# Optimization experiments

Measured on AMD Instinct MI355X. Metric: run time of the kernel, lower is better.

## Reference

```python
import jax, jax.numpy as jnp
import numpy as np

HIDDEN = 1024
HEADS = 16
HEAD_DIM = HIDDEN // HEADS
SCALE = HEAD_DIM ** (-0.5)


def setup_inputs() -> dict:
    key = jax.random.key(0)
    ks = jax.random.split(key, 5)
    B, N, C = 8, 1024, HIDDEN
    x = jax.random.normal(ks[0], (B, N, C), dtype=jnp.float32)
    # torch nn.Linear params: weight [out, in], bias [out]
    w_in = jax.random.normal(ks[1], (3 * C, C), dtype=jnp.float32) * (C ** -0.5)
    b_in = jax.random.normal(ks[2], (3 * C,), dtype=jnp.float32) * 0.02
    w_out = jax.random.normal(ks[3], (C, C), dtype=jnp.float32) * (C ** -0.5)
    b_out = jax.random.normal(ks[4], (C,), dtype=jnp.float32) * 0.02
    return {"x": x, "w_in": w_in, "b_in": b_in, "w_out": w_out, "b_out": b_out}


def reference(x, w_in, b_in, w_out, b_out):
    B, N, C = x.shape
    H, D = HEADS, HEAD_DIM
    # in_proj: [B,N,3C] -> (3,B,H,N,D)
    qkv = x @ w_in.T + b_in
    qkv = qkv.reshape(B, N, 3, H, D).transpose(2, 0, 3, 1, 4)
    q, k, v = qkv[0], qkv[1], qkv[2]
    # attention scores scaled after QK^T (same math as scaling q)
    attn = jnp.einsum("bhnd,bhmd->bhnm", q, k) * SCALE
    attn = jax.nn.softmax(attn, axis=-1)
    out = jnp.einsum("bhnm,bhmd->bhnd", attn, v)  # [B,H,N,D]
    out = out.transpose(0, 2, 1, 3).reshape(B, N, C)
    return out @ w_out.T + b_out
```

## Files before the change

kernel.cpp:

```cpp
#include <hip/hip_runtime.h>


typedef __attribute__((ext_vector_type(8))) __bf16 bf16x8;
typedef __attribute__((ext_vector_type(4))) __bf16 bf16x4;
typedef __attribute__((ext_vector_type(4))) float f32x4;
typedef __attribute__((ext_vector_type(4))) short short4v;

__device__ __forceinline__ f32x4 mfma16(bf16x8 a, bf16x8 b, f32x4 c) {
  return __builtin_amdgcn_mfma_f32_16x16x32_bf16(a, b, c, 0, 0, 0);
}

#if __has_builtin(__builtin_amdgcn_mfma_f32_16x16x16bf16_1k)
__device__ __forceinline__ f32x4 mfma_pv(bf16x4 a, bf16x4 b, f32x4 c) {
  short4v as = __builtin_bit_cast(short4v, a);
  short4v bs = __builtin_bit_cast(short4v, b);
  return __builtin_amdgcn_mfma_f32_16x16x16bf16_1k(as, bs, c, 0, 0, 0);
}
#else
__device__ __forceinline__ f32x4 mfma_pv(bf16x4 a, bf16x4 b, f32x4 c) {
  __bf16 z = (__bf16)0.f;
  bf16x8 a8 = {a[0], a[1], a[2], a[3], z, z, z, z};
  bf16x8 b8 = {b[0], b[1], b[2], b[3], z, z, z, z};
  return mfma16(a8, b8, c);
}
#endif

__device__ __forceinline__ float fexp2(float x) {
#if __has_builtin(__builtin_amdgcn_exp2f)
  return __builtin_amdgcn_exp2f(x);
#else
  return exp2f(x);
#endif
}

typedef __attribute__((address_space(1))) const unsigned int gu32;
typedef __attribute__((address_space(3))) unsigned int lu32;

__device__ __forceinline__ void async16(const void* g, void* l) {
  __builtin_amdgcn_global_load_lds((gu32*)g, (lu32*)l, 16, 0, 0);
}

__global__ __launch_bounds__(256) void cvt_all(const float* __restrict__ x,
                                               __bf16* __restrict__ xb,
                                               const float* __restrict__ wi,
                                               __bf16* __restrict__ wib,
                                               const float* __restrict__ wo,
                                               __bf16* __restrict__ wob) {
  int blk = blockIdx.x;
  const float* in;
  __bf16* out;
  int base;
  if (blk < 4096)      { in = x;  out = xb;  base = 0; }
  else if (blk < 5632) { in = wi; out = wib; base = 4096; }
  else                 { in = wo; out = wob; base = 5632; }
  int i = ((blk - base) * 256 + threadIdx.x) * 8;
  float4 a = *(const float4*)(in + i);
  float4 b = *(const float4*)(in + i + 4);
  bf16x8 o;
  o[0] = (__bf16)a.x; o[1] = (__bf16)a.y; o[2] = (__bf16)a.z; o[3] = (__bf16)a.w;
  o[4] = (__bf16)b.x; o[5] = (__bf16)b.y; o[6] = (__bf16)b.z; o[7] = (__bf16)b.w;
  *(bf16x8*)(out + i) = o;
}

template <int NB, bool WRITE_VT, typename OutT>
__global__ __launch_bounds__(256, 2) void gemm_nt(const __bf16* __restrict__ A,
                                                  const __bf16* __restrict__ Bm,
                                                  const float* __restrict__ bias,
                                                  OutT* __restrict__ C, int K, int ldc,
                                                  __bf16* __restrict__ vt) {
  __shared__ __bf16 As[128 * 32];
  __shared__ __bf16 Bs[NB * 64 * 32];
  const int t = threadIdx.x;
  const int wv = t >> 6, lane = t & 63;
  const int q16 = lane & 15, quad = lane >> 4;
  const int wm = wv >> 1, wn = wv & 1;
  const long m0 = (long)blockIdx.x * 128;
  const long n0 = (long)blockIdx.y * (NB * 32);

  f32x4 zero = {0.f, 0.f, 0.f, 0.f};
  f32x4 acc[4][NB];
#pragma unroll
  for (int i = 0; i < 4; ++i)
#pragma unroll
    for (int j = 0; j < NB; ++j) acc[i][j] = zero;

  char* AsB = (char*)As;
  char* BsB = (char*)Bs;
  const int sr = t >> 2;
  const int cs = t & 3;
  const int gc = cs ^ ((sr >> 1) & 3);

  for (int kt = 0; kt < K; kt += 32) {
    __syncthreads();
    async16(A + (m0 + sr) * K + kt + gc * 8,      AsB + wv * 1024);
    async16(A + (m0 + 64 + sr) * K + kt + gc * 8, AsB + 4096 + wv * 1024);
#pragma unroll
    for (int s = 0; s < NB / 2; ++s)
      async16(Bm + (n0 + s * 64 + sr) * K + kt + gc * 8, BsB + s * 4096 + wv * 1024);
    __syncthreads();

    bf16x8 af[4], bf[NB];
#pragma unroll
    for (int i = 0; i < 4; ++i) {
      int ra = wm * 64 + i * 16 + q16;
      af[i] = *(const bf16x8*)(AsB + ra * 64 + ((quad ^ ((ra >> 1) & 3)) * 16));
    }
#pragma unroll
    for (int j = 0; j < NB; ++j) {
      int rb = wn * (NB * 16) + j * 16 + q16;
      bf[j] = *(const bf16x8*)(BsB + rb * 64 + ((quad ^ ((rb >> 1) & 3)) * 16));
    }
#pragma unroll
    for (int i = 0; i < 4; ++i)
#pragma unroll
      for (int j = 0; j < NB; ++j) acc[i][j] = mfma16(af[i], bf[j], acc[i][j]);
  }

  if (WRITE_VT && n0 >= 2048) {
    const int b = (int)(m0 >> 10);
    const int nbase = (int)(m0 - (long)b * 1024) + wm * 64;
#pragma unroll
    for (int j = 0; j < NB; ++j) {
      int col = (int)n0 + wn * (NB * 16) + j * 16 + q16;
      int cc = col - 2048;
      int h = cc >> 6, d = cc & 63;
      float bs = bias[col];
      __bf16* vrow = vt + (((long)(b * 16 + h)) << 16) + (long)d * 1024;
#pragma unroll
      for (int i = 0; i < 4; ++i) {
        int n = nbase + i * 16 + quad * 4;
        bf16x4 o;
#pragma unroll
        for (int r = 0; r < 4; ++r) o[r] = (__bf16)(acc[i][j][r] + bs);
        *(bf16x4*)(vrow + n) = o;
      }
    }
  } else {
#pragma unroll
    for (int j = 0; j < NB; ++j) {
      long col = n0 + wn * (NB * 16) + j * 16 + q16;
      float bs = bias[col];
#pragma unroll
      for (int i = 0; i < 4; ++i) {
        long rowb = m0 + wm * 64 + i * 16 + quad * 4;
#pragma unroll
        for (int r = 0; r < 4; ++r) {
          float v = acc[i][j][r] + bs;
          C[(rowb + r) * (long)ldc + col] = (OutT)v;
        }
      }
    }
  }
}

__global__ __launch_bounds__(256) void attn_kernel(const __bf16* __restrict__ qkv,
                                                   const __bf16* __restrict__ vt,
                                                   __bf16* __restrict__ ao) {
  __shared__ __bf16 Ks[64 * 64];
  __shared__ __bf16 Vt[64 * 64];
  const int t = threadIdx.x;
  const int wv = t >> 6, lane = t & 63;
  const int q16 = lane & 15, quad = lane >> 4;
  const int bh = blockIdx.x;
  const int b = bh >> 4, h = bh & 15;
  const int q0 = blockIdx.y * 64;
  const long rowbase = (long)b * 1024;

  bf16x8 qf0, qf1;
  {
    long qrow = rowbase + q0 + wv * 16 + q16;
    const __bf16* qp = qkv + qrow * 3072 + h * 64 + quad * 8;
    qf0 = *(const bf16x8*)qp;
    qf1 = *(const bf16x8*)(qp + 32);
#pragma unroll
    for (int j = 0; j < 8; ++j) {
      qf0[j] = (__bf16)((float)qf0[j] * 0.18033688f);
      qf1[j] = (__bf16)((float)qf1[j] * 0.18033688f);
    }
  }

  f32x4 zero = {0.f, 0.f, 0.f, 0.f};
  f32x4 oacc[4];
#pragma unroll
  for (int dt = 0; dt < 4; ++dt) oacc[dt] = zero;
  float lcol = 0.f;

  char* KsB = (char*)Ks;
  char* VtB = (char*)Vt;
  const int sr = t >> 3;
  const int sgc = (t & 7) ^ (sr & 7);
  const int sw = q16 & 7;

  for (int kv0 = 0; kv0 < 1024; kv0 += 64) {
    __syncthreads();
    const __bf16* kg = qkv + (rowbase + kv0 + sr) * 3072 + 1024 + h * 64 + sgc * 8;
    async16(kg, KsB + wv * 1024);
    async16(kg + (long)32 * 3072, KsB + 4096 + wv * 1024);
    const __bf16* vg = vt + (long)bh * 65536 + (long)sr * 1024 + kv0 + sgc * 8;
    async16(vg, VtB + wv * 1024);
    async16(vg + (long)32 * 1024, VtB + 4096 + wv * 1024);
    __syncthreads();

    f32x4 sacc[4];
#pragma unroll
    for (int nt = 0; nt < 4; ++nt) sacc[nt] = zero;
#pragma unroll
    for (int nt = 0; nt < 4; ++nt) {
      int kvr = nt * 16 + q16;
      bf16x8 kf0 = *(const bf16x8*)(KsB + kvr * 128 + ((quad ^ sw) * 16));
      bf16x8 kf1 = *(const bf16x8*)(KsB + kvr * 128 + (((4 + quad) ^ sw) * 16));
      sacc[nt] = mfma16(kf0, qf0, sacc[nt]);
      sacc[nt] = mfma16(kf1, qf1, sacc[nt]);
    }

    bf16x4 pf[4];
#pragma unroll
    for (int nt = 0; nt < 4; ++nt)
#pragma unroll
      for (int r = 0; r < 4; ++r) {
        float p = fexp2(sacc[nt][r]);
        lcol += p;
        pf[nt][r] = (__bf16)p;
      }

#pragma unroll
    for (int nt = 0; nt < 4; ++nt) {
      int c = ((nt * 2 + (quad >> 1)) ^ sw) * 16 + (quad & 1) * 8;
#pragma unroll
      for (int dt = 0; dt < 4; ++dt) {
        bf16x4 vf = *(const bf16x4*)(VtB + (dt * 16 + q16) * 128 + c);
        oacc[dt] = mfma_pv(pf[nt], vf, oacc[dt]);
      }
    }
  }

  lcol += __shfl_xor(lcol, 16);
  lcol += __shfl_xor(lcol, 32);
  float inv = 1.0f / lcol;
#pragma unroll
  for (int r = 0; r < 4; ++r) {
    float ir = __shfl(inv, quad * 4 + r);
    long orow = rowbase + q0 + wv * 16 + quad * 4 + r;
#pragma unroll
    for (int dt = 0; dt < 4; ++dt)
      ao[orow * 1024 + h * 64 + dt * 16 + q16] = (__bf16)(oacc[dt][r] * ir);
  }
}

extern "C" void kernel_launch(void* const* d_in, const int* in_sizes, int n_in,
                              void* d_out, int out_size, void* d_ws, size_t ws_size,
                              hipStream_t stream) {
  const float* x     = (const float*)d_in[0];
  const float* w_in  = (const float*)d_in[1];
  const float* b_in  = (const float*)d_in[2];
  const float* w_out = (const float*)d_in[3];
  const float* b_out = (const float*)d_in[4];
  float* out = (float*)d_out;

  char* ws = (char*)d_ws;
  __bf16* xb   = (__bf16*)(ws);
  __bf16* wib  = (__bf16*)(ws + 16777216);
  __bf16* wob  = (__bf16*)(ws + 23068672);
  __bf16* qkvb = (__bf16*)(ws + 25165824);
  __bf16* aob  = (__bf16*)(ws + 75497472);
  __bf16* vtg  = (__bf16*)d_out;

  cvt_all<<<6144, 256, 0, stream>>>(x, xb, w_in, wib, w_out, wob);
  gemm_nt<8, true, __bf16><<<dim3(64, 12), 256, 0, stream>>>(
      xb, wib, b_in, qkvb, 1024, 3072, vtg);
  attn_kernel<<<dim3(128, 16), 256, 0, stream>>>(qkvb, vtg, aob);
  gemm_nt<4, false, float><<<dim3(64, 8), 256, 0, stream>>>(
      aob, wob, b_out, out, 1024, 1024, nullptr);
}
```

Before: 253.9 us.

## Double-buffer LDS tiles in GEMM and attention kernels to overlap loads

Both the projection GEMM and the attention kernel now use two LDS buffers. The next K or KV tile is issued into the idle buffer while the current one is consumed by MFMAs, and each iteration needs one barrier instead of two. This is meant to hide global-to-LDS load latency behind compute. The cost is twice the shared memory per block, and the GEMM drops its min-blocks-per-CU launch bound, which may lower occupancy.

```diff
diff --git a/kernel.cpp b/kernel.cpp
--- a/kernel.cpp
+++ b/kernel.cpp
@@ -63,13 +63,15 @@
 }
 
 template <int NB, bool WRITE_VT, typename OutT>
-__global__ __launch_bounds__(256, 2) void gemm_nt(const __bf16* __restrict__ A,
-                                                  const __bf16* __restrict__ Bm,
-                                                  const float* __restrict__ bias,
-                                                  OutT* __restrict__ C, int K, int ldc,
-                                                  __bf16* __restrict__ vt) {
-  __shared__ __bf16 As[128 * 32];
-  __shared__ __bf16 Bs[NB * 64 * 32];
+__global__ __launch_bounds__(256) void gemm_nt(const __bf16* __restrict__ A,
+                                               const __bf16* __restrict__ Bm,
+                                               const float* __restrict__ bias,
+                                               OutT* __restrict__ C, int K, int ldc,
+                                               __bf16* __restrict__ vt) {
+  constexpr int ABUF = 8192;
+  constexpr int BBUF = NB * 2048;
+  __shared__ __bf16 As[2 * 4096];
+  __shared__ __bf16 Bs[2 * NB * 1024];
   const int t = threadIdx.x;
   const int wv = t >> 6, lane = t & 63;
   const int q16 = lane & 15, quad = lane >> 4;
@@ -90,25 +92,33 @@
   const int cs = t & 3;
   const int gc = cs ^ ((sr >> 1) & 3);
 
-  for (int kt = 0; kt < K; kt += 32) {
+  auto stage = [&](int buf, int kt) {
+    async16(A + (m0 + sr) * K + kt + gc * 8,      AsB + buf * ABUF + wv * 1024);
+    async16(A + (m0 + 64 + sr) * K + kt + gc * 8, AsB + buf * ABUF + 4096 + wv * 1024);
+#pragma unroll
+    for (int s = 0; s < NB / 2; ++s)
+      async16(Bm + (n0 + s * 64 + sr) * K + kt + gc * 8,
+              BsB + buf * BBUF + s * 4096 + wv * 1024);
+  };
+
+  stage(0, 0);
+  const int T = K >> 5;
+  for (int it = 0; it < T; ++it) {
     __syncthreads();
-    async16(A + (m0 + sr) * K + kt + gc * 8,      AsB + wv * 1024);
-    async16(A + (m0 + 64 + sr) * K + kt + gc * 8, AsB + 4096 + wv * 1024);
-#pragma unroll
-    for (int s = 0; s < NB / 2; ++s)
-      async16(Bm + (n0 + s * 64 + sr) * K + kt + gc * 8, BsB + s * 4096 + wv * 1024);
-    __syncthreads();
+    if (it + 1 < T) stage((it + 1) & 1, (it + 1) << 5);
+    const int bo = (it & 1) ? ABUF : 0;
+    const int bb = (it & 1) ? BBUF : 0;
 
     bf16x8 af[4], bf[NB];
 #pragma unroll
     for (int i = 0; i < 4; ++i) {
       int ra = wm * 64 + i * 16 + q16;
-      af[i] = *(const bf16x8*)(AsB + ra * 64 + ((quad ^ ((ra >> 1) & 3)) * 16));
+      af[i] = *(const bf16x8*)(AsB + bo + ra * 64 + ((quad ^ ((ra >> 1) & 3)) * 16));
     }
 #pragma unroll
     for (int j = 0; j < NB; ++j) {
       int rb = wn * (NB * 16) + j * 16 + q16;
-      bf[j] = *(const bf16x8*)(BsB + rb * 64 + ((quad ^ ((rb >> 1) & 3)) * 16));
+      bf[j] = *(const bf16x8*)(BsB + bb + rb * 64 + ((quad ^ ((rb >> 1) & 3)) * 16));
     }
 #pragma unroll
     for (int i = 0; i < 4; ++i)
@@ -156,8 +166,8 @@
 __global__ __launch_bounds__(256) void attn_kernel(const __bf16* __restrict__ qkv,
                                                    const __bf16* __restrict__ vt,
                                                    __bf16* __restrict__ ao) {
-  __shared__ __bf16 Ks[64 * 64];
-  __shared__ __bf16 Vt[64 * 64];
+  __shared__ __bf16 Ks[2 * 4096];
+  __shared__ __bf16 Vt[2 * 4096];
   const int t = threadIdx.x;
   const int wv = t >> 6, lane = t & 63;
   const int q16 = lane & 15, quad = lane >> 4;
@@ -191,15 +201,20 @@
   const int sgc = (t & 7) ^ (sr & 7);
   const int sw = q16 & 7;
 
-  for (int kv0 = 0; kv0 < 1024; kv0 += 64) {
+  auto stage = [&](int buf, int kv0) {
+    const __bf16* kg = qkv + (rowbase + kv0 + sr) * 3072 + 1024 + h * 64 + sgc * 8;
+    async16(kg, KsB + buf * 8192 + wv * 1024);
+    async16(kg + (long)32 * 3072, KsB + buf * 8192 + 4096 + wv * 1024);
+    const __bf16* vg = vt + (long)bh * 65536 + (long)sr * 1024 + kv0 + sgc * 8;
+    async16(vg, VtB + buf * 8192 + wv * 1024);
+    async16(vg + (long)32 * 1024, VtB + buf * 8192 + 4096 + wv * 1024);
+  };
+
+  stage(0, 0);
+  for (int it = 0; it < 16; ++it) {
     __syncthreads();
-    const __bf16* kg = qkv + (rowbase + kv0 + sr) * 3072 + 1024 + h * 64 + sgc * 8;
-    async16(kg, KsB + wv * 1024);
-    async16(kg + (long)32 * 3072, KsB + 4096 + wv * 1024);
-    const __bf16* vg = vt + (long)bh * 65536 + (long)sr * 1024 + kv0 + sgc * 8;
-    async16(vg, VtB + wv * 1024);
-    async16(vg + (long)32 * 1024, VtB + 4096 + wv * 1024);
-    __syncthreads();
+    if (it + 1 < 16) stage((it + 1) & 1, (it + 1) << 6);
+    const int bo = (it & 1) ? 8192 : 0;
 
     f32x4 sacc[4];
 #pragma unroll
@@ -207,8 +222,8 @@
 #pragma unroll
     for (int nt = 0; nt < 4; ++nt) {
       int kvr = nt * 16 + q16;
-      bf16x8 kf0 = *(const bf16x8*)(KsB + kvr * 128 + ((quad ^ sw) * 16));
-      bf16x8 kf1 = *(const bf16x8*)(KsB + kvr * 128 + (((4 + quad) ^ sw) * 16));
+      bf16x8 kf0 = *(const bf16x8*)(KsB + bo + kvr * 128 + ((quad ^ sw) * 16));
+      bf16x8 kf1 = *(const bf16x8*)(KsB + bo + kvr * 128 + (((4 + quad) ^ sw) * 16));
       sacc[nt] = mfma16(kf0, qf0, sacc[nt]);
       sacc[nt] = mfma16(kf1, qf1, sacc[nt]);
     }
@@ -228,7 +243,7 @@
       int c = ((nt * 2 + (quad >> 1)) ^ sw) * 16 + (quad & 1) * 8;
 #pragma unroll
       for (int dt = 0; dt < 4; ++dt) {
-        bf16x4 vf = *(const bf16x4*)(VtB + (dt * 16 + q16) * 128 + c);
+        bf16x4 vf = *(const bf16x4*)(VtB + bo + (dt * 16 + q16) * 128 + c);
         oacc[dt] = mfma_pv(pf[nt], vf, oacc[dt]);
       }
     }
```

Result: slower. 279.4 us (+10.1%).
